# Kernel optimization log

Hardware: AMD Instinct MI355X
Metric: run time of the kernel (lower is better)

The kernel has to match this reference:

```python
import jax, jax.numpy as jnp
import numpy as np
import math

N_HEADS = 8

def setup_inputs() -> dict:
    key = jax.random.key(0)
    ks = jax.random.split(key, 5)
    B, S, D = 2, 4096, 512
    return {
        "x": jax.random.normal(ks[0], (B, S, D), jnp.float32),
        "W_in": jax.random.normal(ks[1], (D, 3 * D), jnp.float32) * (1.0 / math.sqrt(D)),
        "b_in": jax.random.normal(ks[2], (3 * D,), jnp.float32) * 0.02,
        "W_out": jax.random.normal(ks[3], (D, D), jnp.float32) * (1.0 / math.sqrt(D)),
        "b_out": jax.random.normal(ks[4], (D,), jnp.float32) * 0.02,
        "causal_mask": 1,
    }

def reference(x, W_in, b_in, W_out, b_out, causal_mask):
    B, S, D = x.shape
    H = N_HEADS
    dh = D // H
    qkv = x @ W_in + b_in                      # [B,S,3D]
    q, k, v = jnp.split(qkv, 3, axis=-1)
    # [B,S,D] -> [B,H,S,dh]
    q = q.reshape(B, S, H, dh).transpose(0, 2, 1, 3)
    k = k.reshape(B, S, H, dh).transpose(0, 2, 1, 3)
    v = v.reshape(B, S, H, dh).transpose(0, 2, 1, 3)
    scores = jnp.einsum("bhqd,bhkd->bhqk", q, k)  # [B,H,S,S]
    if causal_mask:
        # strictly upper triangle masked to -inf (before scaling, as in torch code)
        causal = jnp.tril(jnp.ones((S, S), dtype=bool))
        scores = jnp.where(causal, scores, -jnp.inf)
    scores = scores / math.sqrt(dh)
    w = jax.nn.softmax(scores, axis=-1)
    out = jnp.einsum("bhqk,bhkd->bhqd", w, v)     # [B,H,S,dh]
    out = out.transpose(0, 2, 1, 3).reshape(B, S, D)
    return out @ W_out + b_out
```

## Files before the change

kernel.cpp:

```cpp
#include <hip/hip_runtime.h>
#include <stdint.h>

typedef __attribute__((ext_vector_type(8))) short bf16x8;
typedef __attribute__((ext_vector_type(4))) float f32x4;

__device__ __forceinline__ float bf2f(unsigned short b) {
  union { unsigned int u; float f; } c; c.u = ((unsigned int)b) << 16; return c.f;
}
__device__ __forceinline__ unsigned short f2bf(float f) {
  union { float f; unsigned int u; } c; c.f = f;
  unsigned int u = c.u;
  return (unsigned short)((u + 0x7fffu + ((u >> 16) & 1u)) >> 16);
}

__device__ __forceinline__ void gload_lds16(const void* g, void* l) {
  __builtin_amdgcn_global_load_lds((const __attribute__((address_space(1))) void*)g,
                                   (__attribute__((address_space(3))) void*)l,
                                   16, 0, 0);
}

#define QSCALE 0.18033688011112042f


__global__ __launch_bounds__(256) void cvt_x(const float* __restrict__ in,
                                             unsigned short* __restrict__ out, int n4) {
  int i = blockIdx.x * 256 + threadIdx.x;
  if (i < n4) {
    float4 f = ((const float4*)in)[i];
    ushort4 o;
    o.x = f2bf(f.x); o.y = f2bf(f.y); o.z = f2bf(f.z); o.w = f2bf(f.w);
    ((ushort4*)out)[i] = o;
  }
}

__global__ __launch_bounds__(256)
void tw_cvt_t(const float* __restrict__ W, unsigned short* __restrict__ Wt, int N) {
  __shared__ unsigned short T[64][68];
  const int n0 = blockIdx.x * 64, k0 = blockIdx.y * 64;
  const int c = threadIdx.x & 15, r = threadIdx.x >> 4;
#pragma unroll
  for (int i = 0; i < 4; ++i) {
    float4 f = *(const float4*)&W[(size_t)(k0 + i * 16 + r) * N + n0 + c * 4];
    T[c * 4 + 0][i * 16 + r] = f2bf(f.x);
    T[c * 4 + 1][i * 16 + r] = f2bf(f.y);
    T[c * 4 + 2][i * 16 + r] = f2bf(f.z);
    T[c * 4 + 3][i * 16 + r] = f2bf(f.w);
  }
  __syncthreads();
#pragma unroll
  for (int i = 0; i < 4; ++i)
    *(ushort4*)&Wt[(size_t)(n0 + i * 16 + r) * 512 + k0 + c * 4] =
        *(const ushort4*)&T[i * 16 + r][c * 4];
}

__global__ __launch_bounds__(256)
void vtr(const unsigned short* __restrict__ vsd, unsigned short* __restrict__ vt) {
  __shared__ unsigned short T[64][68];
  const int bh = blockIdx.y, s0 = blockIdx.x * 64;
  const int c = threadIdx.x & 15, r = threadIdx.x >> 4;
#pragma unroll
  for (int i = 0; i < 4; ++i) {
    ushort4 u = *(const ushort4*)&vsd[((size_t)bh * 4096 + s0 + i * 16 + r) * 64 + c * 4];
    T[c * 4 + 0][i * 16 + r] = u.x;
    T[c * 4 + 1][i * 16 + r] = u.y;
    T[c * 4 + 2][i * 16 + r] = u.z;
    T[c * 4 + 3][i * 16 + r] = u.w;
  }
  __syncthreads();
#pragma unroll
  for (int i = 0; i < 4; ++i)
    *(ushort4*)&vt[((size_t)bh * 64 + i * 16 + r) * 4096 + s0 + c * 4] =
        *(const ushort4*)&T[i * 16 + r][c * 4];
}


template<int QKV>
__global__ __launch_bounds__(256)
void gemm_bt(const unsigned short* __restrict__ A, const unsigned short* __restrict__ Bt,
             const float* __restrict__ bias, float* __restrict__ Cout,
             unsigned short* __restrict__ qo, unsigned short* __restrict__ ko,
             unsigned short* __restrict__ vo, int M, int N, int K) {
  __shared__ unsigned short As[128 * 64];
  __shared__ unsigned short Bs[128 * 64];
  const int tid = threadIdx.x;
  const int wid = tid >> 6;
  const int lane = tid & 63;
  const int row0 = blockIdx.x * 128;
  const int col0 = blockIdx.y * 128;

  f32x4 acc[4][4];
#pragma unroll
  for (int m = 0; m < 4; ++m)
#pragma unroll
    for (int n = 0; n < 4; ++n)
      acc[m][n] = (f32x4){0.f, 0.f, 0.f, 0.f};

  const int wr = (wid >> 1) * 64;
  const int wc = (wid & 1) * 64;
  const int rw = lane & 15;
  const int nk = K >> 6;

  for (int kt = 0; kt < nk; ++kt) {
    const int k0 = kt << 6;
#pragma unroll
    for (int i = 0; i < 4; ++i) {
      int c = i * 256 + tid;
      int r = c >> 3, kq = (c & 7) << 3;
      gload_lds16(A + (size_t)(row0 + r) * K + k0 + kq, As + (size_t)(i * 256 + wid * 64) * 8);
    }
#pragma unroll
    for (int i = 0; i < 4; ++i) {
      int c = i * 256 + tid;
      int r = c >> 3, kq = (c & 7) << 3;
      gload_lds16(Bt + (size_t)(col0 + r) * K + k0 + kq, Bs + (size_t)(i * 256 + wid * 64) * 8);
    }
    __syncthreads();
#pragma unroll
    for (int ks = 0; ks < 2; ++ks) {
      const int kof = ks * 32 + (lane >> 4) * 8;
      bf16x8 af[4], bfr[4];
#pragma unroll
      for (int m = 0; m < 4; ++m)
        af[m] = *(const bf16x8*)&As[(wr + m * 16 + rw) * 64 + kof];
#pragma unroll
      for (int n = 0; n < 4; ++n)
        bfr[n] = *(const bf16x8*)&Bs[(wc + n * 16 + rw) * 64 + kof];
#pragma unroll
      for (int m = 0; m < 4; ++m)
#pragma unroll
        for (int n = 0; n < 4; ++n)
          acc[m][n] = __builtin_amdgcn_mfma_f32_16x16x32_bf16(af[m], bfr[n], acc[m][n], 0, 0, 0);
    }
    __syncthreads();
  }

  const int lr4 = (lane >> 4) * 4;
  const int lc = lane & 15;
#pragma unroll
  for (int m = 0; m < 4; ++m) {
#pragma unroll
    for (int n = 0; n < 4; ++n) {
      const int col = col0 + wc + n * 16 + lc;
      const float bb = bias[col];
      const int row = row0 + wr + m * 16 + lr4;
      if (QKV) {
        const int which = col >> 9;
        const int rem = col & 511, h = rem >> 6, d = rem & 63;
        const int b = row >> 12, s = row & 4095;
        const float scale = (which == 0) ? QSCALE : 1.0f;
        unsigned short* dst = (which == 0) ? qo : ((which == 1) ? ko : vo);
#pragma unroll
        for (int r2 = 0; r2 < 4; ++r2)
          dst[(((size_t)(b * 8 + h) * 4096 + (s + r2)) << 6) + d] =
              f2bf((acc[m][n][r2] + bb) * scale);
      } else {
#pragma unroll
        for (int r2 = 0; r2 < 4; ++r2)
          Cout[(size_t)(row + r2) * N + col] = acc[m][n][r2] + bb;
      }
    }
  }
}


__global__ __launch_bounds__(64, 3)
void attn_mfma(const unsigned short* __restrict__ Qb, const unsigned short* __restrict__ Kb,
               const unsigned short* __restrict__ Vtb, unsigned short* __restrict__ Ob,
               const int* __restrict__ causal_p) {
  __shared__ unsigned short Ps[32 * 64];

  const int lane = threadIdx.x;
  const int lx = lane & 15, ly = lane >> 4, l7 = lane & 7;
  const int bh = blockIdx.x;
  const int p = 127 - (int)blockIdx.y;
  const int qw = p * 32;
  const int causal = *causal_p;
  const size_t qkbase = (size_t)bh * 4096 * 64;
  const size_t vbase = (size_t)bh * 64 * 4096;

  bf16x8 qf[2][2];
#pragma unroll
  for (int rf = 0; rf < 2; ++rf)
#pragma unroll
    for (int ks = 0; ks < 2; ++ks)
      qf[rf][ks] =
          *(const bf16x8*)(Qb + qkbase + (size_t)(qw + rf * 16 + lx) * 64 + ks * 32 + ly * 8);

  f32x4 o[2][4];
  float mrow[2][4], lpart[2][4];
#pragma unroll
  for (int rf = 0; rf < 2; ++rf) {
#pragma unroll
    for (int df = 0; df < 4; ++df) o[rf][df] = (f32x4){0.f, 0.f, 0.f, 0.f};
#pragma unroll
    for (int r = 0; r < 4; ++r) { mrow[rf][r] = -1e30f; lpart[rf][r] = 0.f; }
  }

  const int ktmax = causal ? ((p * 32 + 31) >> 6) : 63;

  for (int kt = 0; kt <= ktmax; ++kt) {
    const int ktb = kt * 64;

    f32x4 s[2][4];
#pragma unroll
    for (int rf = 0; rf < 2; ++rf)
#pragma unroll
      for (int cf = 0; cf < 4; ++cf) s[rf][cf] = (f32x4){0.f, 0.f, 0.f, 0.f};
#pragma unroll
    for (int ks = 0; ks < 2; ++ks) {
      bf16x8 kf[4];
#pragma unroll
      for (int cf = 0; cf < 4; ++cf)
        kf[cf] = *(const bf16x8*)(Kb + qkbase + (size_t)(ktb + cf * 16 + lx) * 64 +
                                  ks * 32 + ly * 8);
#pragma unroll
      for (int rf = 0; rf < 2; ++rf)
#pragma unroll
        for (int cf = 0; cf < 4; ++cf)
          s[rf][cf] = __builtin_amdgcn_mfma_f32_16x16x32_bf16(qf[rf][ks], kf[cf], s[rf][cf], 0, 0, 0);
    }

    const bool diag = causal && (ktb + 63 > qw);
    float tmx[2][4];
    bool ok = true;
#pragma unroll
    for (int rf = 0; rf < 2; ++rf) {
#pragma unroll
      for (int r = 0; r < 4; ++r) {
        if (diag) {
          const int qg = qw + rf * 16 + ly * 4 + r;
#pragma unroll
          for (int cf = 0; cf < 4; ++cf)
            if (ktb + cf * 16 + lx > qg) s[rf][cf][r] = -1e30f;
        }
        const float a0 = fmaxf(s[rf][0][r], s[rf][1][r]);
        const float a1 = fmaxf(s[rf][2][r], s[rf][3][r]);
        tmx[rf][r] = fmaxf(a0, a1);
        ok = ok && (tmx[rf][r] <= mrow[rf][r] + 8.f);
      }
    }

    if (__all(ok)) {
#pragma unroll
      for (int rf = 0; rf < 2; ++rf) {
#pragma unroll
        for (int r = 0; r < 4; ++r) {
          const float mo = mrow[rf][r];
          const int ql = rf * 16 + ly * 4 + r;
          const int swz = (ql & 7) << 3;
          float lp = 0.f;
#pragma unroll
          for (int cf = 0; cf < 4; ++cf) {
            const float pv = __builtin_amdgcn_exp2f(s[rf][cf][r] - mo);
            lp += pv;
            Ps[ql * 64 + ((cf * 16 + lx) ^ swz)] = f2bf(pv);
          }
          lpart[rf][r] += lp;
        }
      }
    } else {
#pragma unroll
      for (int rf = 0; rf < 2; ++rf) {
#pragma unroll
        for (int r = 0; r < 4; ++r) {
          float tm = tmx[rf][r];
          tm = fmaxf(tm, __shfl_xor(tm, 1));
          tm = fmaxf(tm, __shfl_xor(tm, 2));
          tm = fmaxf(tm, __shfl_xor(tm, 4));
          tm = fmaxf(tm, __shfl_xor(tm, 8));
          const float mo = mrow[rf][r];
          const float mn = fmaxf(mo, tm);
          const float scl = __builtin_amdgcn_exp2f(mo - mn);
          const int ql = rf * 16 + ly * 4 + r;
          const int swz = (ql & 7) << 3;
          float lp = 0.f;
#pragma unroll
          for (int cf = 0; cf < 4; ++cf) {
            const float pv = __builtin_amdgcn_exp2f(s[rf][cf][r] - mn);
            lp += pv;
            Ps[ql * 64 + ((cf * 16 + lx) ^ swz)] = f2bf(pv);
          }
          lpart[rf][r] = lpart[rf][r] * scl + lp;
          mrow[rf][r] = mn;
#pragma unroll
          for (int df = 0; df < 4; ++df) o[rf][df][r] *= scl;
        }
      }
    }

#pragma unroll
    for (int ks = 0; ks < 2; ++ks) {
      const int kel = ((ks * 4 + ly) ^ l7) << 3;
      bf16x8 pa[2], vf[4];
#pragma unroll
      for (int rf = 0; rf < 2; ++rf)
        pa[rf] = *(const bf16x8*)&Ps[(rf * 16 + lx) * 64 + kel];
#pragma unroll
      for (int df = 0; df < 4; ++df)
        vf[df] = *(const bf16x8*)(Vtb + vbase + (size_t)(df * 16 + lx) * 4096 +
                                  ktb + ks * 32 + ly * 8);
#pragma unroll
      for (int rf = 0; rf < 2; ++rf)
#pragma unroll
        for (int df = 0; df < 4; ++df)
          o[rf][df] = __builtin_amdgcn_mfma_f32_16x16x32_bf16(pa[rf], vf[df], o[rf][df], 0, 0, 0);
    }
  }

  const int b = bh >> 3, h = bh & 7;
#pragma unroll
  for (int rf = 0; rf < 2; ++rf) {
#pragma unroll
    for (int r = 0; r < 4; ++r) {
      float l = lpart[rf][r];
      l += __shfl_xor(l, 1);
      l += __shfl_xor(l, 2);
      l += __shfl_xor(l, 4);
      l += __shfl_xor(l, 8);
      const float inv = 1.0f / l;
      const int row = b * 4096 + qw + rf * 16 + ly * 4 + r;
#pragma unroll
      for (int df = 0; df < 4; ++df)
        Ob[(size_t)row * 512 + h * 64 + df * 16 + lx] = f2bf(o[rf][df][r] * inv);
    }
  }
}


extern "C" void kernel_launch(void* const* d_in, const int* in_sizes, int n_in,
                              void* d_out, int out_size, void* d_ws, size_t ws_size,
                              hipStream_t stream) {
  const float* x     = (const float*)d_in[0];
  const float* W_in  = (const float*)d_in[1];
  const float* b_in  = (const float*)d_in[2];
  const float* W_out = (const float*)d_in[3];
  const float* b_out = (const float*)d_in[4];
  const int* causal  = (const int*)d_in[5];
  float* out = (float*)d_out;

  unsigned short* xb   = (unsigned short*)d_ws;
  unsigned short* wint = xb + 4194304;
  unsigned short* wout = wint + 786432;
  unsigned short* qb   = wout + 262144;
  unsigned short* kb   = qb + 4194304;
  unsigned short* vt   = kb + 4194304;
  unsigned short* vsd  = (unsigned short*)d_out;

  cvt_x<<<4096, 256, 0, stream>>>(x, xb, 1048576);
  tw_cvt_t<<<dim3(24, 8), 256, 0, stream>>>(W_in, wint, 1536);
  tw_cvt_t<<<dim3(8, 8), 256, 0, stream>>>(W_out, wout, 512);

  gemm_bt<1><<<dim3(64, 12), 256, 0, stream>>>(xb, wint, b_in, nullptr, qb, kb, vsd,
                                               8192, 1536, 512);

  vtr<<<dim3(64, 16), 256, 0, stream>>>(vsd, vt);

  attn_mfma<<<dim3(16, 128), 64, 0, stream>>>(qb, kb, vt, xb, causal);

  gemm_bt<0><<<dim3(64, 4), 256, 0, stream>>>(xb, wout, b_out, out, nullptr, nullptr, nullptr,
                                              8192, 512, 512);
}
```

Before: 387.5 us.

## Split attention key range across four waves per block with LDS merge

Each attention block now runs four waves, and each wave processes a contiguous quarter of the causal key tiles for the same 32 query rows (split-K flash attention). Per-wave partial outputs, running maxima and sums are staged in LDS and combined after a barrier, with a vectorized store at the end. This targets the serial key loop and the load imbalance from causal masking, where late query blocks have up to 64 tiles and early ones only one. In exchange it adds LDS traffic, a barrier and a merge step. Partial outputs are rounded to bf16 before the merge, and short rows leave some waves idle.

Result: slower. 663.7 us (+71.3%).

```diff
diff --git a/kernel.cpp b/kernel.cpp
--- a/kernel.cpp
+++ b/kernel.cpp
@@ -163,13 +163,16 @@
 }
 
 
-__global__ __launch_bounds__(64, 3)
+__global__ __launch_bounds__(256, 5)
 void attn_mfma(const unsigned short* __restrict__ Qb, const unsigned short* __restrict__ Kb,
                const unsigned short* __restrict__ Vtb, unsigned short* __restrict__ Ob,
                const int* __restrict__ causal_p) {
-  __shared__ unsigned short Ps[32 * 64];
-
-  const int lane = threadIdx.x;
+  __shared__ unsigned short Ps[4][32 * 64];
+  __shared__ float mlds[4][2][32];
+
+  const int tid = threadIdx.x;
+  const int wid = tid >> 6;
+  const int lane = tid & 63;
   const int lx = lane & 15, ly = lane >> 4, l7 = lane & 7;
   const int bh = blockIdx.x;
   const int p = 127 - (int)blockIdx.y;
@@ -178,6 +181,11 @@
   const size_t qkbase = (size_t)bh * 4096 * 64;
   const size_t vbase = (size_t)bh * 64 * 4096;
 
+  const int ktmax = causal ? ((qw + 31) >> 6) : 63;
+  const int Q4 = (ktmax + 4) >> 2;
+  const int kt0 = wid * Q4;
+  const int ktend = min(ktmax, kt0 + Q4 - 1);
+
   bf16x8 qf[2][2];
 #pragma unroll
   for (int rf = 0; rf < 2; ++rf)
@@ -196,9 +204,7 @@
     for (int r = 0; r < 4; ++r) { mrow[rf][r] = -1e30f; lpart[rf][r] = 0.f; }
   }
 
-  const int ktmax = causal ? ((p * 32 + 31) >> 6) : 63;
-
-  for (int kt = 0; kt <= ktmax; ++kt) {
+  for (int kt = kt0; kt <= ktend; ++kt) {
     const int ktb = kt * 64;
 
     f32x4 s[2][4];
@@ -253,7 +259,7 @@
           for (int cf = 0; cf < 4; ++cf) {
             const float pv = __builtin_amdgcn_exp2f(s[rf][cf][r] - mo);
             lp += pv;
-            Ps[ql * 64 + ((cf * 16 + lx) ^ swz)] = f2bf(pv);
+            Ps[wid][ql * 64 + ((cf * 16 + lx) ^ swz)] = f2bf(pv);
           }
           lpart[rf][r] += lp;
         }
@@ -278,7 +284,7 @@
           for (int cf = 0; cf < 4; ++cf) {
             const float pv = __builtin_amdgcn_exp2f(s[rf][cf][r] - mn);
             lp += pv;
-            Ps[ql * 64 + ((cf * 16 + lx) ^ swz)] = f2bf(pv);
+            Ps[wid][ql * 64 + ((cf * 16 + lx) ^ swz)] = f2bf(pv);
           }
           lpart[rf][r] = lpart[rf][r] * scl + lp;
           mrow[rf][r] = mn;
@@ -294,7 +300,7 @@
       bf16x8 pa[2], vf[4];
 #pragma unroll
       for (int rf = 0; rf < 2; ++rf)
-        pa[rf] = *(const bf16x8*)&Ps[(rf * 16 + lx) * 64 + kel];
+        pa[rf] = *(const bf16x8*)&Ps[wid][(rf * 16 + lx) * 64 + kel];
 #pragma unroll
       for (int df = 0; df < 4; ++df)
         vf[df] = *(const bf16x8*)(Vtb + vbase + (size_t)(df * 16 + lx) * 4096 +
@@ -307,7 +313,6 @@
     }
   }
 
-  const int b = bh >> 3, h = bh & 7;
 #pragma unroll
   for (int rf = 0; rf < 2; ++rf) {
 #pragma unroll
@@ -317,13 +322,42 @@
       l += __shfl_xor(l, 2);
       l += __shfl_xor(l, 4);
       l += __shfl_xor(l, 8);
-      const float inv = 1.0f / l;
-      const int row = b * 4096 + qw + rf * 16 + ly * 4 + r;
+      const int rloc = rf * 16 + ly * 4 + r;
+      if (lx == 0) {
+        mlds[wid][0][rloc] = mrow[rf][r];
+        mlds[wid][1][rloc] = l;
+      }
 #pragma unroll
       for (int df = 0; df < 4; ++df)
-        Ob[(size_t)row * 512 + h * 64 + df * 16 + lx] = f2bf(o[rf][df][r] * inv);
-    }
-  }
+        Ps[wid][rloc * 64 + df * 16 + lx] = f2bf(o[rf][df][r]);
+    }
+  }
+  __syncthreads();
+
+  const int b = bh >> 3, h = bh & 7;
+  const int row = tid >> 3;
+  const int c0 = (tid & 7) * 8;
+  float M = -1e30f;
+#pragma unroll
+  for (int w = 0; w < 4; ++w) M = fmaxf(M, mlds[w][0][row]);
+  float sc[4], L = 0.f;
+#pragma unroll
+  for (int w = 0; w < 4; ++w) {
+    sc[w] = __builtin_amdgcn_exp2f(mlds[w][0][row] - M);
+    L += mlds[w][1][row] * sc[w];
+  }
+  const float inv = 1.0f / L;
+  unsigned short res[8];
+#pragma unroll
+  for (int j = 0; j < 8; ++j) {
+    float O = 0.f;
+#pragma unroll
+    for (int w = 0; w < 4; ++w) O += bf2f(Ps[w][row * 64 + c0 + j]) * sc[w];
+    res[j] = f2bf(O * inv);
+  }
+  const size_t base = (size_t)(b * 4096 + qw + row) * 512 + h * 64 + c0;
+  *(ushort4*)&Ob[base] = (ushort4){res[0], res[1], res[2], res[3]};
+  *(ushort4*)&Ob[base + 4] = (ushort4){res[4], res[5], res[6], res[7]};
 }
 
 
@@ -355,7 +389,7 @@
 
   vtr<<<dim3(64, 16), 256, 0, stream>>>(vsd, vt);
 
-  attn_mfma<<<dim3(16, 128), 64, 0, stream>>>(qb, kb, vt, xb, causal);
+  attn_mfma<<<dim3(16, 128), 256, 0, stream>>>(qb, kb, vt, xb, causal);
 
   gemm_bt<0><<<dim3(64, 4), 256, 0, stream>>>(xb, wout, b_out, out, nullptr, nullptr, nullptr,
                                               8192, 512, 512);
```
